# Performance work log

Hardware: AMD Instinct MI355X
Metric: run time of the kernel (lower is better)

## Reference

```python
import jax, jax.numpy as jnp
import numpy as np

V, WD, H, B, S, A = 50000, 300, 300, 64, 128, 8
H2 = 2 * H
NEG = -1e9


def _reverse_padded(x, lens):
    # reverse each sequence within its valid length; zeros elsewhere
    T = x.shape[1]
    idx = lens[:, None] - 1 - jnp.arange(T)[None, :]          # [B,T]
    valid = (idx >= 0)
    idx = jnp.clip(idx, 0, T - 1)
    return jnp.take_along_axis(x, idx[:, :, None], axis=1) * valid[:, :, None]


def _lstm_dir(x, lens, Wih, Whh, bih, bhh):
    # single-direction LSTM; emulates pack_padded: state frozen and output 0 past lens
    Bn, T, _ = x.shape
    Hn = Whh.shape[1]
    h0 = jnp.zeros((Bn, Hn), x.dtype)
    valid = (jnp.arange(T)[None, :] < lens[:, None]).astype(x.dtype)  # [B,T]

    def step(carry, inp):
        h, c = carry
        xt, vt = inp                                          # xt [B,D], vt [B,1]
        g = xt @ Wih.T + bih + h @ Whh.T + bhh                # [B,4H]
        i, f, gg, o = jnp.split(g, 4, axis=-1)                # torch gate order i,f,g,o
        i = jax.nn.sigmoid(i); f = jax.nn.sigmoid(f)
        o = jax.nn.sigmoid(o); gg = jnp.tanh(gg)
        c_new = f * c + i * gg
        h_new = o * jnp.tanh(c_new)
        h = vt * h_new + (1.0 - vt) * h
        c = vt * c_new + (1.0 - vt) * c
        return (h, c), vt * h_new

    _, outs = jax.lax.scan(step, (h0, h0), (x.transpose(1, 0, 2), valid.T[:, :, None]))
    return outs.transpose(1, 0, 2)                            # [B,T,H]


def _bilstm(x, lens, Wih, Whh, bih, bhh):
    fwd = _lstm_dir(x, lens, Wih[0], Whh[0], bih[0], bhh[0])
    xr = _reverse_padded(x, lens)
    bwd = _lstm_dir(xr, lens, Wih[1], Whh[1], bih[1], bhh[1])
    bwd = _reverse_padded(bwd, lens)
    return jnp.concatenate([fwd, bwd], axis=-1)               # [B,T,2H]


def setup_inputs() -> dict:
    key = jax.random.key(0)
    ks = jax.random.split(key, 16)
    lens_t = jax.random.randint(ks[0], (B,), S // 2, S + 1)
    ids_t = jax.random.randint(ks[1], (B, S), 1, V)
    text = jnp.where(jnp.arange(S)[None, :] < lens_t[:, None], ids_t, 0)
    lens_a = jax.random.randint(ks[2], (B,), 2, A + 1)
    ids_a = jax.random.randint(ks[3], (B, A), 1, V)
    aspect_ids = jnp.where(jnp.arange(A)[None, :] < lens_a[:, None], ids_a, 0)
    position_weight = jax.random.uniform(ks[4], (B, S), jnp.float32) * (text != 0)
    s = 0.05
    emb = jax.random.normal(ks[5], (V, WD), jnp.float32) * s
    emb = emb.at[0].set(0.0)  # padding row

    def lstm_params(k):
        k1, k2, k3, k4 = jax.random.split(k, 4)
        return (jax.random.normal(k1, (2, 4 * H, WD), jnp.float32) * s,
                jax.random.normal(k2, (2, 4 * H, H), jnp.float32) * s,
                jax.random.normal(k3, (2, 4 * H), jnp.float32) * s,
                jax.random.normal(k4, (2, 4 * H), jnp.float32) * s)

    l1_Wih, l1_Whh, l1_bih, l1_bhh = lstm_params(ks[6])
    l2_Wih, l2_Whh, l2_bih, l2_bhh = lstm_params(ks[7])
    return dict(
        text=text, aspect_ids=aspect_ids, position_weight=position_weight, emb=emb,
        l1_Wih=l1_Wih, l1_Whh=l1_Whh, l1_bih=l1_bih, l1_bhh=l1_bhh,
        l2_Wih=l2_Wih, l2_Whh=l2_Whh, l2_bih=l2_bih, l2_bhh=l2_bhh,
        lin1_W=jax.random.normal(ks[8], (2, H2, 2 * H2), jnp.float32) * s,
        lin1_b=jax.random.normal(ks[9], (2, H2), jnp.float32) * s,
        lin2_W=jax.random.normal(ks[10], (2, 1, H2), jnp.float32) * s,
        lin2_b=jax.random.normal(ks[11], (2, 1), jnp.float32) * s,
        fc_W=jax.random.normal(ks[12], (3, H2), jnp.float32) * s,
        fc_b=jax.random.normal(ks[13], (3,), jnp.float32) * s,
    )


def reference(text, aspect_ids, position_weight, emb,
              l1_Wih, l1_Whh, l1_bih, l1_bhh,
              l2_Wih, l2_Whh, l2_bih, l2_bhh,
              lin1_W, lin1_b, lin2_W, lin2_b, fc_W, fc_b):
    text_len = jnp.sum(text != 0, axis=-1)
    asp_len = jnp.sum(aspect_ids != 0, axis=-1)
    masks = (text != 0).astype(jnp.float32)          # [B,S]
    tmasks = (aspect_ids != 0).astype(jnp.float32)   # [B,A]
    wf = emb[text]                                    # [B,S,WD]
    af = emb[aspect_ids]                              # [B,A,WD]
    v = _bilstm(wf, text_len, l1_Wih, l1_Whh, l1_bih, l1_bhh)   # [B,S,2H]
    e = _bilstm(af, asp_len, l2_Wih, l2_Whh, l2_bih, l2_bhh)    # [B,A,2H]
    pair_mask = masks[:, :, None] * tmasks[:, None, :]          # [B,S,A]
    for i in range(2):
        a = jnp.einsum('bsd,bad->bsa', v, e)
        a = jnp.where(pair_mask == 0, NEG, a)
        a = jax.nn.softmax(a, axis=2)
        mid = jnp.einsum('bsa,bad->bsd', a, e)                  # [B,S,2H]
        mid = jnp.concatenate([mid, v], axis=-1)                # [B,S,4H]
        mid = jax.nn.leaky_relu(mid @ lin1_W[i].T + lin1_b[i])  # [B,S,2H]
        t = jax.nn.sigmoid(v @ lin2_W[i].T + lin2_b[i])         # [B,S,1]
        v = (1.0 - t) * mid + t * v
        v = position_weight[:, :, None] * v
    e_masked = jnp.where(tmasks[:, :, None] == 0, NEG, e)
    query = jnp.max(e_masked, axis=1)                           # [B,2H]
    alpha = jnp.einsum('bsd,bd->bs', v, query)
    alpha = jnp.where(masks == 0, NEG, alpha)
    alpha = jax.nn.softmax(alpha, axis=1)
    z = jnp.einsum('bs,bsd->bd', alpha, v)                      # [B,2H]
    return z @ fc_W.T + fc_b                                    # [B,3]
```

## Files before the change

kernel.cpp:

```cpp
#include <hip/hip_runtime.h>
#include <hip/hip_bf16.h>
#include <hip/hip_fp16.h>


typedef unsigned short u16;
typedef __attribute__((ext_vector_type(8))) short short8;
typedef __attribute__((ext_vector_type(4))) float floatx4;

#define NEGV -1e9f
#define MFMA __builtin_amdgcn_mfma_f32_16x16x32_bf16

__device__ __forceinline__ float bf2f(u16 u) {
    union { unsigned int i; float f; } x; x.i = ((unsigned int)u) << 16; return x.f;
}
__device__ __forceinline__ u16 f2bf(float f) {
    unsigned int u = __float_as_uint(f);
    unsigned int r = (u + 0x7fff + ((u >> 16) & 1)) >> 16;
    return (u16)r;
}
__device__ __forceinline__ float h16(u16 u) {
    __half h; *(u16*)&h = u; return __half2float(h);
}
__device__ __forceinline__ u16 f16(float f) {
    __half h = __float2half(f); return *(u16*)&h;
}
__device__ __forceinline__ float sigm(float x) { return 1.f / (1.f + expf(-x)); }
__device__ __forceinline__ float rdf(const void* p, size_t i, int flag) {
    return flag ? ((const float*)p)[i] : bf2f(((const u16*)p)[i]);
}

#if defined(__has_builtin)
# if __has_builtin(__builtin_amdgcn_fdot2)
#  define USE_FDOT2_BUILTIN 1
# endif
#endif
typedef __attribute__((ext_vector_type(2))) _Float16 half2v;
__device__ __forceinline__ float dot2f(unsigned int w, unsigned int h, float acc) {
#ifdef USE_FDOT2_BUILTIN
    union { unsigned int u; half2v v; } a, b;
    a.u = w; b.u = h;
    return __builtin_amdgcn_fdot2(a.v, b.v, acc, false);
#else
    asm("v_dot2_f32_f16 %0, %1, %2, %0" : "+v"(acc) : "v"(w), "v"(h));
    return acc;
#endif
}

__global__ void k_detect(const void* __restrict__ emb, int* __restrict__ flag) {
    __shared__ int cnt;
    if (threadIdx.x == 0) cnt = 0;
    __syncthreads();
    u16 x = ((const u16*)emb)[4096 + threadIdx.x];
    int e = (x >> 7) & 0xFF;
    if (e >= 0x8A) atomicAdd(&cnt, 1);
    __syncthreads();
    if (threadIdx.x == 0) *flag = (cnt > 8) ? 1 : 0;
}

__global__ void k_prep_small(const int* __restrict__ text, const int* __restrict__ asp,
                             int* __restrict__ lens) {
    int tid = threadIdx.x;
    if (tid < 64) {
        int c = 0;
        for (int s = 0; s < 128; ++s) c += (text[tid * 128 + s] != 0);
        lens[tid] = c;
    } else if (tid < 128) {
        int b = tid - 64; int c = 0;
        for (int a = 0; a < 8; ++a) c += (asp[b * 8 + a] != 0);
        lens[64 + b] = c;
    }
}

__global__ void k_pad_wih2(const void* __restrict__ W1, const void* __restrict__ W2,
                           const int* __restrict__ flag,
                           u16* __restrict__ d1h, u16* __restrict__ d1l,
                           u16* __restrict__ d2h, u16* __restrict__ d2l) {
    int i = blockIdx.x * 256 + threadIdx.x;
    if (i >= 2 * 2432 * 320) return;
    int f = *flag;
    int layer = i / (2432 * 320), r = i - layer * (2432 * 320);
    int n = r / 320, k = r - n * 320;
    const void* W = layer ? W2 : W1;
    float val = (n < 2400 && k < 300) ? rdf(W, (size_t)n * 300 + k, f) : 0.f;
    u16 hi = f2bf(val);
    float lo = val - bf2f(hi);
    if (layer) { d2h[r] = hi; d2l[r] = f2bf(lo); }
    else       { d1h[r] = hi; d1l[r] = f2bf(lo); }
}

__global__ void k_whhT2(const void* __restrict__ W1, const void* __restrict__ W2,
                        const int* __restrict__ flag,
                        u16* __restrict__ d1, u16* __restrict__ d2) {
    int i = blockIdx.x * 256 + threadIdx.x;
    if (i >= 2 * 720000) return;
    int f = *flag;
    int layer = i / 720000, r = i - layer * 720000;
    int dir = r / 360000, rr = r - dir * 360000;
    int kp = rr / 2400, t = rr - kp * 2400;
    int cc = t >> 1, j = t & 1;
    int k = 2 * kp + j;
    const void* W = layer ? W2 : W1;
    u16 bits = f16(rdf(W, (size_t)dir * 360000 + (size_t)cc * 300 + k, f));
    if (layer) d2[r] = bits; else d1[r] = bits;
}

__global__ void k_pad_lin1AB(const void* __restrict__ W, const int* __restrict__ flag,
                             u16* __restrict__ Ahi, u16* __restrict__ Alo,
                             u16* __restrict__ Bhi, u16* __restrict__ Blo) {
    int i = blockIdx.x * 256 + threadIdx.x;
    if (i >= 2 * 640 * 608) return;
    int f = *flag;
    int it = i / (640 * 608), r = i - it * (640 * 608);
    int n = r / 608, k = r - n * 608;
    float va = 0.f, vb = 0.f;
    if (n < 600 && k < 600) {
        va = rdf(W, (size_t)it * 720000 + (size_t)n * 1200 + k, f);
        vb = rdf(W, (size_t)it * 720000 + (size_t)n * 1200 + 600 + k, f);
    }
    u16 h;
    h = f2bf(va); Ahi[i] = h; Alo[i] = f2bf(va - bf2f(h));
    h = f2bf(vb); Bhi[i] = h; Blo[i] = f2bf(vb - bf2f(h));
}

__global__ void k_esplit(const float* __restrict__ e,
                         u16* __restrict__ ehi, u16* __restrict__ elo) {
    int i = blockIdx.x * 256 + threadIdx.x;
    if (i >= 512 * 608) return;
    int r = i / 608, k = i - r * 608;
    float val = (k < 600) ? e[r * 600 + k] : 0.f;
    u16 h = f2bf(val);
    ehi[i] = h;
    elo[i] = f2bf(val - bf2f(h));
}

__global__ void k_small(const void* pw, const void* l2w, const void* l2b,
                        const void* fcw, const void* fcb, const void* lb,
                        const void* b1i, const void* b1h, const void* b2i, const void* b2h,
                        const int* __restrict__ flag,
                        float* __restrict__ dst, float* __restrict__ bl,
                        float* __restrict__ bt, float* __restrict__ ba) {
    int i = blockIdx.x * 256 + threadIdx.x;
    int f = *flag;
    if (i < 8192)            dst[i] = rdf(pw, i, f);
    else if (i < 9392)       dst[i] = rdf(l2w, i - 8192, f);
    else if (i < 9394)       dst[i] = rdf(l2b, i - 9392, f);
    else if (i < 11194)      dst[i] = rdf(fcw, i - 9394, f);
    else if (i < 11197)      dst[i] = rdf(fcb, i - 11194, f);
    if (i < 1280) {
        int dir = i / 640, c = i - dir * 640;
        bl[i] = (c < 600) ? rdf(lb, dir * 600 + c, f) : 0.f;
    }
    if (i < 2400) {
        bt[i] = rdf(b1i, i, f) + rdf(b1h, i, f);
        ba[i] = rdf(b2i, i, f) + rdf(b2h, i, f);
    }
}

__device__ __forceinline__ void gemm_emb_tile(
    const void* __restrict__ emb, const int* __restrict__ ids,
    int base, int rpb, int stride, int f,
    const u16* __restrict__ Bhi, const u16* __restrict__ Blo,
    const float* __restrict__ bias,
    u16* __restrict__ C, int ldc, int nstore, int bx, int by, int tid)
{
    int wave = tid >> 6, lane = tid & 63;
    int l15 = lane & 15, quad = lane >> 4;
    int m0 = bx * 64 + wave * 16;
    int n0 = by * 64;

    int m = m0 + l15;
    int b = m / rpb, j = m - b * rpb;
    int id = ids[b * stride + base + j];
    const float* arow_f = (const float*)emb + (size_t)id * 300;
    const u16*   arow_b = (const u16*)emb + (size_t)id * 300;

    const u16* Bp  = Bhi + (size_t)(n0 + l15) * 320 + quad * 8;
    const u16* Bp2 = Blo + (size_t)(n0 + l15) * 320 + quad * 8;

    floatx4 acc0 = {0.f, 0.f, 0.f, 0.f};
    floatx4 acc1 = acc0, acc2 = acc0, acc3 = acc0;

    for (int kc = 0; kc < 10; ++kc) {
        int ko = kc * 32 + quad * 8;
        short8 ahi, alo;
        if (f) {
            if (ko + 8 <= 300) {
                float4 fa = *(const float4*)(arow_f + ko);
                float4 fb = *(const float4*)(arow_f + ko + 4);
                float vv[8] = {fa.x, fa.y, fa.z, fa.w, fb.x, fb.y, fb.z, fb.w};
                #pragma unroll
                for (int t = 0; t < 8; ++t) {
                    u16 h = f2bf(vv[t]);
                    ahi[t] = (short)h;
                    alo[t] = (short)f2bf(vv[t] - bf2f(h));
                }
            } else {
                #pragma unroll
                for (int t = 0; t < 8; ++t) {
                    int k = ko + t;
                    float vv = (k < 300) ? arow_f[k] : 0.f;
                    u16 h = f2bf(vv);
                    ahi[t] = (short)h;
                    alo[t] = (short)f2bf(vv - bf2f(h));
                }
            }
        } else {
            #pragma unroll
            for (int t = 0; t < 8; ++t) {
                int k = ko + t;
                ahi[t] = (k < 300) ? (short)arow_b[k] : (short)0;
                alo[t] = 0;
            }
        }
        int ko2 = kc * 32;
        short8 bh0 = *(const short8*)(Bp + ko2);
        short8 bh1 = *(const short8*)(Bp + (size_t)16 * 320 + ko2);
        short8 bh2 = *(const short8*)(Bp + (size_t)32 * 320 + ko2);
        short8 bh3 = *(const short8*)(Bp + (size_t)48 * 320 + ko2);
        short8 bl0 = *(const short8*)(Bp2 + ko2);
        short8 bl1 = *(const short8*)(Bp2 + (size_t)16 * 320 + ko2);
        short8 bl2 = *(const short8*)(Bp2 + (size_t)32 * 320 + ko2);
        short8 bl3 = *(const short8*)(Bp2 + (size_t)48 * 320 + ko2);
        acc0 = MFMA(ahi, bh0, acc0, 0, 0, 0);
        acc1 = MFMA(ahi, bh1, acc1, 0, 0, 0);
        acc2 = MFMA(ahi, bh2, acc2, 0, 0, 0);
        acc3 = MFMA(ahi, bh3, acc3, 0, 0, 0);
        acc0 = MFMA(ahi, bl0, acc0, 0, 0, 0);
        acc1 = MFMA(ahi, bl1, acc1, 0, 0, 0);
        acc2 = MFMA(ahi, bl2, acc2, 0, 0, 0);
        acc3 = MFMA(ahi, bl3, acc3, 0, 0, 0);
        acc0 = MFMA(alo, bh0, acc0, 0, 0, 0);
        acc1 = MFMA(alo, bh1, acc1, 0, 0, 0);
        acc2 = MFMA(alo, bh2, acc2, 0, 0, 0);
        acc3 = MFMA(alo, bh3, acc3, 0, 0, 0);
    }

    #pragma unroll
    for (int c = 0; c < 4; ++c) {
        floatx4 acc = (c == 0) ? acc0 : (c == 1) ? acc1 : (c == 2) ? acc2 : acc3;
        int col = n0 + c * 16 + l15;
        if (col >= nstore) continue;
        float bb = bias[col];
        #pragma unroll
        for (int r = 0; r < 4; ++r) {
            int row = m0 + quad * 4 + r;
            C[(size_t)row * ldc + col] = f16(acc[r] + bb);
        }
    }
}

__global__ __launch_bounds__(256) void gemm_embk(
    const void* __restrict__ emb, const int* __restrict__ ids,
    int base, int rpb, int stride, const int* __restrict__ flag,
    const u16* __restrict__ Bhi, const u16* __restrict__ Blo,
    const float* __restrict__ bias,
    u16* __restrict__ C, int ldc, int nstore)
{
    gemm_emb_tile(emb, ids, base, rpb, stride, *flag, Bhi, Blo, bias,
                  C, ldc, nstore, blockIdx.x, blockIdx.y, threadIdx.x);
}

__device__ __forceinline__ void gemm_core(
    const u16* __restrict__ Ap, const u16* __restrict__ Ap2,
    const u16* __restrict__ Bp, const u16* __restrict__ Bp2,
    int lda, int ldb, int nk,
    floatx4& acc0, floatx4& acc1, floatx4& acc2, floatx4& acc3)
{
    for (int kc = 0; kc < nk; ++kc) {
        int ko = kc * 32;
        short8 bh0 = *(const short8*)(Bp + ko);
        short8 bh1 = *(const short8*)(Bp + (size_t)16 * ldb + ko);
        short8 bh2 = *(const short8*)(Bp + (size_t)32 * ldb + ko);
        short8 bh3 = *(const short8*)(Bp + (size_t)48 * ldb + ko);
        short8 bl0 = *(const short8*)(Bp2 + ko);
        short8 bl1 = *(const short8*)(Bp2 + (size_t)16 * ldb + ko);
        short8 bl2 = *(const short8*)(Bp2 + (size_t)32 * ldb + ko);
        short8 bl3 = *(const short8*)(Bp2 + (size_t)48 * ldb + ko);
        short8 a  = *(const short8*)(Ap + ko);
        short8 al = *(const short8*)(Ap2 + ko);
        acc0 = MFMA(a, bh0, acc0, 0, 0, 0);
        acc1 = MFMA(a, bh1, acc1, 0, 0, 0);
        acc2 = MFMA(a, bh2, acc2, 0, 0, 0);
        acc3 = MFMA(a, bh3, acc3, 0, 0, 0);
        acc0 = MFMA(a, bl0, acc0, 0, 0, 0);
        acc1 = MFMA(a, bl1, acc1, 0, 0, 0);
        acc2 = MFMA(a, bl2, acc2, 0, 0, 0);
        acc3 = MFMA(a, bl3, acc3, 0, 0, 0);
        acc0 = MFMA(al, bh0, acc0, 0, 0, 0);
        acc1 = MFMA(al, bh1, acc1, 0, 0, 0);
        acc2 = MFMA(al, bh2, acc2, 0, 0, 0);
        acc3 = MFMA(al, bh3, acc3, 0, 0, 0);
    }
}

__global__ __launch_bounds__(256) void gemm_ew(
    const u16* __restrict__ Ahi, const u16* __restrict__ Alo,
    const u16* __restrict__ l1a_hi, const u16* __restrict__ l1a_lo,
    float* __restrict__ EW)
{
    int tid = threadIdx.x;
    int wave = tid >> 6, lane = tid & 63;
    int l15 = lane & 15, quad = lane >> 4;
    int iter = blockIdx.z;
    int m0 = blockIdx.x * 64 + wave * 16;
    int n0 = blockIdx.y * 64;
    const u16* Ap  = Ahi + (size_t)(m0 + l15) * 608 + quad * 8;
    const u16* Ap2 = Alo + (size_t)(m0 + l15) * 608 + quad * 8;
    const u16* Bp  = l1a_hi + (size_t)iter * 640 * 608 + (size_t)(n0 + l15) * 608 + quad * 8;
    const u16* Bp2 = l1a_lo + (size_t)iter * 640 * 608 + (size_t)(n0 + l15) * 608 + quad * 8;
    floatx4 acc0 = {0.f, 0.f, 0.f, 0.f};
    floatx4 acc1 = acc0, acc2 = acc0, acc3 = acc0;
    gemm_core(Ap, Ap2, Bp, Bp2, 608, 608, 19, acc0, acc1, acc2, acc3);
    #pragma unroll
    for (int c = 0; c < 4; ++c) {
        floatx4 acc = (c == 0) ? acc0 : (c == 1) ? acc1 : (c == 2) ? acc2 : acc3;
        int col = n0 + c * 16 + l15;
        if (col >= 600) continue;
        #pragma unroll
        for (int r = 0; r < 4; ++r) {
            int row = m0 + quad * 4 + r;
            EW[((size_t)iter * 512 + row) * 600 + col] = acc[r];
        }
    }
}

__global__ __launch_bounds__(256) void gemm_vt(
    const u16* __restrict__ vhi, const u16* __restrict__ vlo,
    const u16* __restrict__ Bhi, const u16* __restrict__ Blo,
    const float* __restrict__ bias,
    const float* __restrict__ EW, const float* __restrict__ a_sm,
    const float* __restrict__ tg, const float* __restrict__ pw,
    float* __restrict__ vio)
{
    __shared__ float al_s[64][8];
    __shared__ float ew_s[8][64];
    int tid = threadIdx.x;
    int wave = tid >> 6, lane = tid & 63;
    int l15 = lane & 15, quad = lane >> 4;
    int m0 = blockIdx.x * 64 + wave * 16;
    int n0 = blockIdx.y * 64;
    int row0 = blockIdx.x * 64;
    int bidx = row0 >> 7;

    for (int i = tid; i < 512; i += 256)
        al_s[i >> 3][i & 7] = a_sm[(size_t)(row0 + (i >> 3)) * 8 + (i & 7)];
    for (int i = tid; i < 512; i += 256) {
        int a = i >> 6, cc = i & 63;
        int col = n0 + cc;
        ew_s[a][cc] = (col < 600) ? EW[((size_t)bidx * 8 + a) * 600 + col] : 0.f;
    }
    __syncthreads();

    const u16* Ap  = vhi + (size_t)(m0 + l15) * 608 + quad * 8;
    const u16* Ap2 = vlo + (size_t)(m0 + l15) * 608 + quad * 8;
    const u16* Bp  = Bhi + (size_t)(n0 + l15) * 608 + quad * 8;
    const u16* Bp2 = Blo + (size_t)(n0 + l15) * 608 + quad * 8;
    floatx4 acc0 = {0.f, 0.f, 0.f, 0.f};
    floatx4 acc1 = acc0, acc2 = acc0, acc3 = acc0;
    gemm_core(Ap, Ap2, Bp, Bp2, 608, 608, 19, acc0, acc1, acc2, acc3);

    #pragma unroll
    for (int c = 0; c < 4; ++c) {
        floatx4 acc = (c == 0) ? acc0 : (c == 1) ? acc1 : (c == 2) ? acc2 : acc3;
        int cc = c * 16 + l15;
        int col = n0 + cc;
        if (col >= 600) continue;
        float bb = bias[col];
        #pragma unroll
        for (int r = 0; r < 4; ++r) {
            int rr = wave * 16 + quad * 4 + r;
            int row = row0 + rr;
            float mid = 0.f;
            #pragma unroll
            for (int a = 0; a < 8; ++a) mid += al_s[rr][a] * ew_s[a][cc];
            float val = acc[r] + bb + mid;
            val = val > 0.f ? val : 0.01f * val;
            float t = tg[row];
            size_t vi = (size_t)row * 600 + col;
            float vv = vio[vi];
            vio[vi] = pw[row] * ((1.f - t) * val + t * vv);
        }
    }
}

__global__ __launch_bounds__(960, 1) void k_lstm6(
    const u16* __restrict__ xf, const u16* __restrict__ xb, int ldx, int rpb,
    int base_f, int base_b, const u16* __restrict__ whhT,
    const int* __restrict__ lens, float* __restrict__ out, int T, int init,
    float* __restrict__ hst, float* __restrict__ cst, int nsteps,
    const u16* __restrict__ xa, const u16* __restrict__ whhA,
    const int* __restrict__ lensA, float* __restrict__ outA,
    float* __restrict__ hstA, float* __restrict__ cstA, int nLstm,
    const void* __restrict__ emb, const int* __restrict__ text,
    int bf_next, int bb_next, const int* __restrict__ flag,
    const u16* __restrict__ wih_hi, const u16* __restrict__ wih_lo,
    const float* __restrict__ bias_t,
    u16* __restrict__ xf_next, u16* __restrict__ xb_next)
{
    __shared__ float part[6][1200];
    __shared__ u16 wlds[6][4][2400];
    __shared__ __align__(4) u16 hs16[304];
    int blk = blockIdx.x;
    if (blk >= nLstm) {
        if (threadIdx.x >= 256) return;
        int g = blk - nLstm;
        int dirn = g / 608; int t = g - dirn * 608;
        int bx = t & 31, by = t >> 5;
        gemm_emb_tile(emb, text, dirn ? bb_next : bf_next, 32, 128, *flag,
                      wih_hi + (dirn ? 1200ull * 320 : 0),
                      wih_lo + (dirn ? 1200ull * 320 : 0),
                      bias_t + (dirn ? 1200 : 0),
                      dirn ? xb_next : xf_next, 1200, 1200, bx, by, threadIdx.x);
        return;
    }
    if (blk >= 128) {
        blk -= 128;
        xf = xa; xb = xa + 1200; ldx = 2400; rpb = 8;
        base_f = 0; base_b = 0;
        whhT = whhA; lens = lensA; out = outA; T = 8; init = 1;
        hst = hstA; cst = cstA; nsteps = 8;
    }
    int tid = threadIdx.x;
    int g6 = tid / 160, u = tid - g6 * 160;
    bool act = (u < 150);
    int b = blk >> 1, dir = blk & 1;
    int len = lens[b];
    float c = 0.f, hf = 0.f;
    const u16* wbase = whhT + (size_t)dir * 360000 + (size_t)g6 * 60000 + 16 * u;

    uint4 wA[8], wB[8];
    if (act) {
        #pragma unroll
        for (int r = 0; r < 8; ++r) {
            wA[r] = *(const uint4*)(wbase + (size_t)r * 2400);
            wB[r] = *(const uint4*)(wbase + (size_t)r * 2400 + 8);
        }
        #pragma unroll
        for (int r = 0; r < 4; ++r) {
            *(uint4*)&wlds[g6][r][16 * u]     = *(const uint4*)(wbase + (size_t)(8 + r) * 2400);
            *(uint4*)&wlds[g6][r][16 * u + 8] = *(const uint4*)(wbase + (size_t)(8 + r) * 2400 + 8);
        }
    }
    if (tid < 300) {
        hf = init ? 0.f : hst[(size_t)blk * 300 + tid];
        c  = init ? 0.f : cst[(size_t)blk * 300 + tid];
        hs16[tid] = f16(hf);
    }
    __syncthreads();
    const u16* wstream = wbase + (size_t)12 * 2400;

    for (int s = 0; s < nsteps; ++s) {
        int pos = dir ? (base_b + nsteps - 1 - s) : (base_f + s);
        if (pos >= len) continue;
        if (act) {
            float a0 = 0.f, a1 = 0.f, a2 = 0.f, a3 = 0.f;
            float a4 = 0.f, a5 = 0.f, a6 = 0.f, a7 = 0.f;
            const unsigned int* h2p = (const unsigned int*)(hs16 + g6 * 50);
            #define DOT8(va, vb, hh)                                   \
                a0 = dot2f((va).x, hh, a0); a1 = dot2f((va).y, hh, a1);\
                a2 = dot2f((va).z, hh, a2); a3 = dot2f((va).w, hh, a3);\
                a4 = dot2f((vb).x, hh, a4); a5 = dot2f((vb).y, hh, a5);\
                a6 = dot2f((vb).z, hh, a6); a7 = dot2f((vb).w, hh, a7);
            #pragma unroll
            for (int r = 0; r < 8; ++r) {
                unsigned int h2 = h2p[r];
                DOT8(wA[r], wB[r], h2);
            }
            #pragma unroll
            for (int r = 0; r < 4; ++r) {
                unsigned int h2 = h2p[8 + r];
                uint4 va = *(const uint4*)&wlds[g6][r][16 * u];
                uint4 vb = *(const uint4*)&wlds[g6][r][16 * u + 8];
                DOT8(va, vb, h2);
            }
            const u16* wp = wstream;
            #pragma unroll 4
            for (int i = 0; i < 13; ++i) {
                unsigned int h2 = h2p[12 + i];
                uint4 va = *(const uint4*)wp;
                uint4 vb = *(const uint4*)(wp + 8);
                wp += 2400;
                DOT8(va, vb, h2);
            }
            #undef DOT8
            float* pp = &part[g6][8 * u];
            float4 w0 = {a0, a1, a2, a3};
            float4 w1 = {a4, a5, a6, a7};
            *(float4*)pp = w0;
            *(float4*)(pp + 4) = w1;
        }
        __syncthreads();
        if (tid < 300) {
            const u16* xr = dir ? (xb + (size_t)(b * rpb + pos - base_b) * ldx)
                                : (xf + (size_t)(b * rpb + pos - base_f) * ldx);
            float gi = h16(xr[tid]), gf = h16(xr[300 + tid]);
            float gg = h16(xr[600 + tid]), go = h16(xr[900 + tid]);
            #pragma unroll
            for (int g = 0; g < 6; ++g) {
                gi += part[g][tid];
                gf += part[g][300 + tid];
                gg += part[g][600 + tid];
                go += part[g][900 + tid];
            }
            gi = sigm(gi); gf = sigm(gf); gg = tanhf(gg); go = sigm(go);
            c = gf * c + gi * gg;
            float hn = go * tanhf(c);
            out[((size_t)b * T + pos) * 600 + dir * 300 + tid] = hn;
            hf = hn;
            hs16[tid] = f16(hn);
        }
        __syncthreads();
    }
    if (tid < 300) {
        hst[(size_t)blk * 300 + tid] = hf;
        cst[(size_t)blk * 300 + tid] = c;
    }
}

__global__ __launch_bounds__(128) void k_scorev(
    const float* __restrict__ v, const float* __restrict__ e,
    const int* __restrict__ text, const int* __restrict__ asp,
    const float* __restrict__ l2w, const float* __restrict__ l2b, int iter,
    float* __restrict__ a_sm, float* __restrict__ tg,
    u16* __restrict__ vhi, u16* __restrict__ vlo)
{
    __shared__ float vs[600];
    __shared__ float red[2][9];
    int row = blockIdx.x;
    int b = row >> 7;
    int t = threadIdx.x, wv = t >> 6, lane = t & 63;
    const float* vrow = v + (size_t)row * 600;
    const float* eb = e + (size_t)b * 4800;
    const float* w2 = l2w + iter * 600;

    for (int d = t; d < 600; d += 128) vs[d] = vrow[d];
    __syncthreads();

    float acc[9];
    #pragma unroll
    for (int j = 0; j < 9; ++j) acc[j] = 0.f;
    for (int d = t; d < 600; d += 128) {
        float vv = vs[d];
        #pragma unroll
        for (int a = 0; a < 8; ++a) acc[a] += vv * eb[a * 600 + d];
        acc[8] += vv * w2[d];
    }
    #pragma unroll
    for (int off = 32; off >= 1; off >>= 1) {
        #pragma unroll
        for (int j = 0; j < 9; ++j) acc[j] += __shfl_down(acc[j], off, 64);
    }
    if (lane == 0) {
        #pragma unroll
        for (int j = 0; j < 9; ++j) red[wv][j] = acc[j];
    }
    __syncthreads();
    if (t == 0) {
        float dots[9];
        #pragma unroll
        for (int j = 0; j < 9; ++j) dots[j] = red[0][j] + red[1][j];
        tg[row] = sigm(dots[8] + l2b[iter]);
        bool sm = (text[row] != 0);
        float sc[8]; float mx = -INFINITY;
        #pragma unroll
        for (int a = 0; a < 8; ++a) {
            sc[a] = (sm && asp[b * 8 + a] != 0) ? dots[a] : NEGV;
            mx = fmaxf(mx, sc[a]);
        }
        float den = 0.f;
        #pragma unroll
        for (int a = 0; a < 8; ++a) { sc[a] = expf(sc[a] - mx); den += sc[a]; }
        float inv = 1.f / den;
        #pragma unroll
        for (int a = 0; a < 8; ++a) a_sm[(size_t)row * 8 + a] = sc[a] * inv;
    }
    for (int d = t; d < 608; d += 128) {
        float val = (d < 600) ? vs[d] : 0.f;
        u16 h = f2bf(val);
        vhi[(size_t)row * 608 + d] = h;
        vlo[(size_t)row * 608 + d] = f2bf(val - bf2f(h));
    }
}

__global__ void k_query(const float* __restrict__ e, const int* __restrict__ asp,
                        float* __restrict__ q) {
    int i = blockIdx.x * 256 + threadIdx.x;
    if (i >= 64 * 600) return;
    int b = i / 600, d = i - b * 600;
    float m = NEGV;
    for (int a = 0; a < 8; ++a)
        if (asp[b * 8 + a] != 0) m = fmaxf(m, e[(size_t)b * 4800 + a * 600 + d]);
    q[i] = m;
}

__global__ __launch_bounds__(128) void k_final(
    const float* __restrict__ v, const float* __restrict__ q,
    const int* __restrict__ text, const float* __restrict__ fcW,
    const float* __restrict__ fcb, const int* __restrict__ flag, void* __restrict__ outv)
{
    __shared__ float red[128];
    __shared__ float al[128];
    __shared__ float zz[600];
    int b = blockIdx.x, s = threadIdx.x;
    const float* vrow = v + (size_t)(b * 128 + s) * 600;
    const float* qb = q + (size_t)b * 600;
    float sc = 0.f;
    for (int d = 0; d < 600; ++d) sc += vrow[d] * qb[d];
    if (text[b * 128 + s] == 0) sc = NEGV;
    red[s] = sc; __syncthreads();
    for (int off = 64; off >= 1; off >>= 1) {
        if (s < off) red[s] = fmaxf(red[s], red[s + off]);
        __syncthreads();
    }
    float mx = red[0]; __syncthreads();
    float ex = expf(sc - mx);
    red[s] = ex; __syncthreads();
    for (int off = 64; off >= 1; off >>= 1) {
        if (s < off) red[s] += red[s + off];
        __syncthreads();
    }
    float alpha = ex / red[0];
    al[s] = alpha; __syncthreads();
    for (int d = s; d < 600; d += 128) {
        float z = 0.f;
        for (int s2 = 0; s2 < 128; ++s2) z += al[s2] * v[(size_t)(b * 128 + s2) * 600 + d];
        zz[d] = z;
    }
    __syncthreads();
    if (s < 3) {
        float o = 0.f;
        for (int d = 0; d < 600; ++d) o += zz[d] * fcW[s * 600 + d];
        o += fcb[s];
        if (*flag) ((float*)outv)[b * 3 + s] = o;
        else       ((u16*)outv)[b * 3 + s] = f2bf(o);
    }
}

extern "C" void kernel_launch(void* const* d_in, const int* in_sizes, int n_in,
                              void* d_out, int out_size, void* d_ws, size_t ws_size,
                              hipStream_t stream) {
    const int*  text   = (const int*)d_in[0];
    const int*  asp    = (const int*)d_in[1];
    const void* pw     = d_in[2];
    const void* emb    = d_in[3];
    const void* l1_Wih = d_in[4];
    const void* l1_Whh = d_in[5];
    const void* l1_bih = d_in[6];
    const void* l1_bhh = d_in[7];
    const void* l2_Wih = d_in[8];
    const void* l2_Whh = d_in[9];
    const void* l2_bih = d_in[10];
    const void* l2_bhh = d_in[11];
    const void* lin1_W = d_in[12];
    const void* lin1_b = d_in[13];
    const void* lin2_W = d_in[14];
    const void* lin2_b = d_in[15];
    const void* fcW    = d_in[16];
    const void* fcb    = d_in[17];
    (void)ws_size; (void)n_in; (void)in_sizes; (void)out_size;

    char* w = (char*)d_ws;
    size_t off = 0;
    auto alloc = [&](size_t bytes) -> void* {
        void* p = w + off;
        off += (bytes + 255) & ~(size_t)255;
        return p;
    };
    int*   flag     = (int*)  alloc(4);
    int*   lens     = (int*)  alloc(128ull * 4);
    float* bias_t   = (float*)alloc(2400ull * 4);
    float* bias_a   = (float*)alloc(2400ull * 4);
    float* bias_l1  = (float*)alloc(1280ull * 4);
    float* smallf   = (float*)alloc(11197ull * 4);
    float* tg       = (float*)alloc(8192ull * 4);
    float* a_sm     = (float*)alloc(8192ull * 8 * 4);
    float* query    = (float*)alloc(64ull * 600 * 4);
    float* hst_t    = (float*)alloc(128ull * 300 * 4);
    float* cst_t    = (float*)alloc(128ull * 300 * 4);
    float* hst_a    = (float*)alloc(128ull * 300 * 4);
    float* cst_a    = (float*)alloc(128ull * 300 * 4);
    float* e        = (float*)alloc(512ull * 600 * 4);
    float* v        = (float*)alloc(8192ull * 600 * 4);
    float* pw_f     = smallf;
    float* l2w_f    = smallf + 8192;
    float* l2b_f    = smallf + 9392;
    float* fcW_f    = smallf + 9394;
    float* fcb_f    = smallf + 11194;
    size_t phase_off = off;
    u16*   wiht_hi  = (u16*)  alloc(2432ull * 320 * 2);
    u16*   wiht_lo  = (u16*)  alloc(2432ull * 320 * 2);
    u16*   wiha_hi  = (u16*)  alloc(2432ull * 320 * 2);
    u16*   wiha_lo  = (u16*)  alloc(2432ull * 320 * 2);
    u16*   whhT_t   = (u16*)  alloc(720000ull * 2);
    u16*   whhT_a   = (u16*)  alloc(720000ull * 2);
    u16*   xf0      = (u16*)  alloc(2048ull * 1200 * 2);
    u16*   xb0      = (u16*)  alloc(2048ull * 1200 * 2);
    u16*   xf1      = (u16*)  alloc(2048ull * 1200 * 2);
    u16*   xb1      = (u16*)  alloc(2048ull * 1200 * 2);
    u16*   xproj_a  = (u16*)  alloc(512ull * 2400 * 2);
    off = phase_off;
    u16*   l1a_hi   = (u16*)  alloc(2ull * 640 * 608 * 2);
    u16*   l1a_lo   = (u16*)  alloc(2ull * 640 * 608 * 2);
    u16*   l1b_hi   = (u16*)  alloc(2ull * 640 * 608 * 2);
    u16*   l1b_lo   = (u16*)  alloc(2ull * 640 * 608 * 2);
    u16*   ehi      = (u16*)  alloc(512ull * 608 * 2);
    u16*   elo      = (u16*)  alloc(512ull * 608 * 2);
    float* EW       = (float*)alloc(2ull * 512 * 600 * 4);
    u16*   vhi      = (u16*)  alloc(8192ull * 608 * 2);
    u16*   vlo      = (u16*)  alloc(8192ull * 608 * 2);

    hipMemsetAsync(v, 0, 8192ull * 600 * 4, stream);
    hipMemsetAsync(e, 0, 512ull * 600 * 4, stream);

    k_detect<<<1, 256, 0, stream>>>(emb, flag);
    k_prep_small<<<1, 128, 0, stream>>>(text, asp, lens);
    k_pad_wih2<<<(2 * 2432 * 320 + 255) / 256, 256, 0, stream>>>(
        l1_Wih, l2_Wih, flag, wiht_hi, wiht_lo, wiha_hi, wiha_lo);
    k_whhT2<<<(2 * 720000 + 255) / 256, 256, 0, stream>>>(
        l1_Whh, l2_Whh, flag, whhT_t, whhT_a);
    k_small<<<49, 256, 0, stream>>>(pw, lin2_W, lin2_b, fcW, fcb, lin1_b,
                                    l1_bih, l1_bhh, l2_bih, l2_bhh, flag,
                                    smallf, bias_l1, bias_t, bias_a);

    gemm_embk<<<dim3(8, 38), 256, 0, stream>>>(emb, asp, 0, 8, 8, flag,
        wiha_hi, wiha_lo, bias_a, xproj_a, 2400, 2400);
    gemm_embk<<<dim3(32, 19), 256, 0, stream>>>(emb, text, 0, 32, 128, flag,
        wiht_hi, wiht_lo, bias_t, xf0, 1200, 1200);
    gemm_embk<<<dim3(32, 19), 256, 0, stream>>>(emb, text, 96, 32, 128, flag,
        wiht_hi + 1200ull * 320, wiht_lo + 1200ull * 320, bias_t + 1200,
        xb0, 1200, 1200);

    for (int kk = 0; kk < 4; ++kk) {
        int bf = 32 * kk;
        int bb = 96 - 32 * kk;
        u16* xfc = (kk & 1) ? xf1 : xf0;
        u16* xbc = (kk & 1) ? xb1 : xb0;
        u16* xfn = (kk & 1) ? xf0 : xf1;
        u16* xbn = (kk & 1) ? xb0 : xb1;
        int nLstm = (kk == 0) ? 256 : 128;
        int haveNext = (kk < 3);
        int nblk = nLstm + (haveNext ? 1216 : 0);
        k_lstm6<<<nblk, 960, 0, stream>>>(xfc, xbc, 1200, 32, bf, bb,
            whhT_t, lens, v, 128, kk == 0 ? 1 : 0, hst_t, cst_t, 32,
            xproj_a, whhT_a, lens + 64, e, hst_a, cst_a, nLstm,
            emb, text, bf + 32, bb - 32, flag, wiht_hi, wiht_lo, bias_t,
            xfn, xbn);
    }

    k_pad_lin1AB<<<(2 * 640 * 608 + 255) / 256, 256, 0, stream>>>(
        lin1_W, flag, l1a_hi, l1a_lo, l1b_hi, l1b_lo);
    k_esplit<<<(512 * 608 + 255) / 256, 256, 0, stream>>>(e, ehi, elo);
    gemm_ew<<<dim3(8, 10, 2), 256, 0, stream>>>(ehi, elo, l1a_hi, l1a_lo, EW);

    for (int iter = 0; iter < 2; ++iter) {
        k_scorev<<<8192, 128, 0, stream>>>(v, e, text, asp, l2w_f, l2b_f,
            iter, a_sm, tg, vhi, vlo);
        gemm_vt<<<dim3(128, 10), 256, 0, stream>>>(vhi, vlo,
            l1b_hi + (size_t)iter * 640 * 608, l1b_lo + (size_t)iter * 640 * 608,
            bias_l1 + iter * 640, EW + (size_t)iter * 512 * 600,
            a_sm, tg, pw_f, v);
    }

    k_query<<<150, 256, 0, stream>>>(e, asp, query);
    k_final<<<64, 128, 0, stream>>>(v, query, text, fcW_f, fcb_f, flag, d_out);
}
```

Before: 1.102 ms.

## Hold recurrent weights in AGPRs and split LDS tiles into bank-friendly halves

Moves the register-resident slice of the LSTM recurrent weights from VGPRs into accumulation registers using explicit accvgpr write/read instructions. It shrinks that slice from 8 to 6 rows and lets the streamed global part grow from 13 to 15 rows, now issued before the register and LDS parts. It also splits the LDS weight tile and the partial-sum buffer into two 8-byte-strided halves to reduce bank conflicts, with a remapped index in the gate reduction. The aim is to ease VGPR pressure and LDS conflicts, but it adds more global weight traffic each step and extra accvgpr read instructions.

New measurement: 1.137 ms. +3.1%, slower.

```diff
diff --git a/kernel.cpp b/kernel.cpp
--- a/kernel.cpp
+++ b/kernel.cpp
@@ -397,8 +397,8 @@
     const float* __restrict__ bias_t,
     u16* __restrict__ xf_next, u16* __restrict__ xb_next)
 {
-    __shared__ float part[6][1200];
-    __shared__ u16 wlds[6][4][2400];
+    __shared__ float part2[6][2][600];
+    __shared__ u16 wlds[6][4][2][1200];
     __shared__ __align__(4) u16 hs16[304];
     int blk = blockIdx.x;
     if (blk >= nLstm) {
@@ -428,17 +428,25 @@
     float c = 0.f, hf = 0.f;
     const u16* wbase = whhT + (size_t)dir * 360000 + (size_t)g6 * 60000 + 16 * u;
 
-    uint4 wA[8], wB[8];
+    uint4 agA[6], agB[6];
+    #pragma unroll
+    for (int r = 0; r < 6; ++r) {
+        uint4 t0 = *(const uint4*)(wbase + (size_t)r * 2400);
+        uint4 t1 = *(const uint4*)(wbase + (size_t)r * 2400 + 8);
+        asm volatile("v_accvgpr_write_b32 %0, %1" : "=a"(agA[r].x) : "v"(t0.x));
+        asm volatile("v_accvgpr_write_b32 %0, %1" : "=a"(agA[r].y) : "v"(t0.y));
+        asm volatile("v_accvgpr_write_b32 %0, %1" : "=a"(agA[r].z) : "v"(t0.z));
+        asm volatile("v_accvgpr_write_b32 %0, %1" : "=a"(agA[r].w) : "v"(t0.w));
+        asm volatile("v_accvgpr_write_b32 %0, %1" : "=a"(agB[r].x) : "v"(t1.x));
+        asm volatile("v_accvgpr_write_b32 %0, %1" : "=a"(agB[r].y) : "v"(t1.y));
+        asm volatile("v_accvgpr_write_b32 %0, %1" : "=a"(agB[r].z) : "v"(t1.z));
+        asm volatile("v_accvgpr_write_b32 %0, %1" : "=a"(agB[r].w) : "v"(t1.w));
+    }
     if (act) {
         #pragma unroll
-        for (int r = 0; r < 8; ++r) {
-            wA[r] = *(const uint4*)(wbase + (size_t)r * 2400);
-            wB[r] = *(const uint4*)(wbase + (size_t)r * 2400 + 8);
-        }
-        #pragma unroll
         for (int r = 0; r < 4; ++r) {
-            *(uint4*)&wlds[g6][r][16 * u]     = *(const uint4*)(wbase + (size_t)(8 + r) * 2400);
-            *(uint4*)&wlds[g6][r][16 * u + 8] = *(const uint4*)(wbase + (size_t)(8 + r) * 2400 + 8);
+            *(uint4*)&wlds[g6][r][0][8 * u] = *(const uint4*)(wbase + (size_t)(6 + r) * 2400);
+            *(uint4*)&wlds[g6][r][1][8 * u] = *(const uint4*)(wbase + (size_t)(6 + r) * 2400 + 8);
         }
     }
     if (tid < 300) {
@@ -446,8 +454,12 @@
         c  = init ? 0.f : cst[(size_t)blk * 300 + tid];
         hs16[tid] = f16(hf);
     }
+    int gc0 = tid,       gh0 = (gc0 >> 2) & 1, gi0 = ((gc0 >> 3) << 2) | (gc0 & 3);
+    int gc1 = 300 + tid, gh1 = (gc1 >> 2) & 1, gi1 = ((gc1 >> 3) << 2) | (gc1 & 3);
+    int gc2 = 600 + tid, gh2 = (gc2 >> 2) & 1, gi2 = ((gc2 >> 3) << 2) | (gc2 & 3);
+    int gc3 = 900 + tid, gh3 = (gc3 >> 2) & 1, gi3 = ((gc3 >> 3) << 2) | (gc3 & 3);
     __syncthreads();
-    const u16* wstream = wbase + (size_t)12 * 2400;
+    const u16* wstream = wbase + (size_t)10 * 2400;
 
     for (int s = 0; s < nsteps; ++s) {
         int pos = dir ? (base_b + nsteps - 1 - s) : (base_f + s);
@@ -461,33 +473,41 @@
                 a2 = dot2f((va).z, hh, a2); a3 = dot2f((va).w, hh, a3);\
                 a4 = dot2f((vb).x, hh, a4); a5 = dot2f((vb).y, hh, a5);\
                 a6 = dot2f((vb).z, hh, a6); a7 = dot2f((vb).w, hh, a7);
-            #pragma unroll
-            for (int r = 0; r < 8; ++r) {
-                unsigned int h2 = h2p[r];
-                DOT8(wA[r], wB[r], h2);
-            }
-            #pragma unroll
-            for (int r = 0; r < 4; ++r) {
-                unsigned int h2 = h2p[8 + r];
-                uint4 va = *(const uint4*)&wlds[g6][r][16 * u];
-                uint4 vb = *(const uint4*)&wlds[g6][r][16 * u + 8];
-                DOT8(va, vb, h2);
-            }
             const u16* wp = wstream;
-            #pragma unroll 4
-            for (int i = 0; i < 13; ++i) {
-                unsigned int h2 = h2p[12 + i];
+            #pragma unroll 5
+            for (int i = 0; i < 15; ++i) {
+                unsigned int h2 = h2p[10 + i];
                 uint4 va = *(const uint4*)wp;
                 uint4 vb = *(const uint4*)(wp + 8);
                 wp += 2400;
                 DOT8(va, vb, h2);
             }
+            #pragma unroll
+            for (int r = 0; r < 6; ++r) {
+                unsigned int h2 = h2p[r];
+                uint4 va, vb;
+                asm("v_accvgpr_read_b32 %0, %1" : "=v"(va.x) : "a"(agA[r].x));
+                asm("v_accvgpr_read_b32 %0, %1" : "=v"(va.y) : "a"(agA[r].y));
+                asm("v_accvgpr_read_b32 %0, %1" : "=v"(va.z) : "a"(agA[r].z));
+                asm("v_accvgpr_read_b32 %0, %1" : "=v"(va.w) : "a"(agA[r].w));
+                asm("v_accvgpr_read_b32 %0, %1" : "=v"(vb.x) : "a"(agB[r].x));
+                asm("v_accvgpr_read_b32 %0, %1" : "=v"(vb.y) : "a"(agB[r].y));
+                asm("v_accvgpr_read_b32 %0, %1" : "=v"(vb.z) : "a"(agB[r].z));
+                asm("v_accvgpr_read_b32 %0, %1" : "=v"(vb.w) : "a"(agB[r].w));
+                DOT8(va, vb, h2);
+            }
+            #pragma unroll
+            for (int r = 0; r < 4; ++r) {
+                unsigned int h2 = h2p[6 + r];
+                uint4 va = *(const uint4*)&wlds[g6][r][0][8 * u];
+                uint4 vb = *(const uint4*)&wlds[g6][r][1][8 * u];
+                DOT8(va, vb, h2);
+            }
             #undef DOT8
-            float* pp = &part[g6][8 * u];
             float4 w0 = {a0, a1, a2, a3};
             float4 w1 = {a4, a5, a6, a7};
-            *(float4*)pp = w0;
-            *(float4*)(pp + 4) = w1;
+            *(float4*)&part2[g6][0][4 * u] = w0;
+            *(float4*)&part2[g6][1][4 * u] = w1;
         }
         __syncthreads();
         if (tid < 300) {
@@ -497,10 +517,10 @@
             float gg = h16(xr[600 + tid]), go = h16(xr[900 + tid]);
             #pragma unroll
             for (int g = 0; g < 6; ++g) {
-                gi += part[g][tid];
-                gf += part[g][300 + tid];
-                gg += part[g][600 + tid];
-                go += part[g][900 + tid];
+                gi += part2[g][gh0][gi0];
+                gf += part2[g][gh1][gi1];
+                gg += part2[g][gh2][gi2];
+                go += part2[g][gh3][gi3];
             }
             gi = sigm(gi); gf = sigm(gf); gg = tanhf(gg); go = sigm(go);
             c = gf * c + gi * gg;
```

## Store recurrent LSTM weights as scaled FP8 and keep more in LDS

Applied to the files above, without the earlier changes.

Recurrent Whh weights are quantized to FP8 (e4m3) with a 64x scale instead of fp16, halving their footprint. The register-held weight slices are dropped; 8 rows now sit in LDS and the rest stream from global, with dot products done via fp8-to-f32 unpack plus FMAs against an fp32 hidden state scaled by 1/64. This cuts weight bandwidth and register pressure in the sequential recurrence, but FP8 greatly lowers accuracy, and the unpack-plus-FMA path costs more ALU work than packed fp16 dot2.

Result: slower. 1.389 ms (+26.0%).

```diff
diff --git a/kernel.cpp b/kernel.cpp
--- a/kernel.cpp
+++ b/kernel.cpp
@@ -6,6 +6,7 @@
 typedef unsigned short u16;
 typedef __attribute__((ext_vector_type(8))) short short8;
 typedef __attribute__((ext_vector_type(4))) float floatx4;
+typedef __attribute__((ext_vector_type(2))) float floatx2;
 
 #define NEGV -1e9f
 #define MFMA __builtin_amdgcn_mfma_f32_16x16x32_bf16
@@ -30,19 +31,49 @@
 }
 
 #if defined(__has_builtin)
-# if __has_builtin(__builtin_amdgcn_fdot2)
-#  define USE_FDOT2_BUILTIN 1
+# if __has_builtin(__builtin_amdgcn_cvt_pk_f32_fp8) && __has_builtin(__builtin_amdgcn_cvt_pk_fp8_f32)
+#  define USE_CVT_FP8 1
 # endif
 #endif
-typedef __attribute__((ext_vector_type(2))) _Float16 half2v;
-__device__ __forceinline__ float dot2f(unsigned int w, unsigned int h, float acc) {
-#ifdef USE_FDOT2_BUILTIN
-    union { unsigned int u; half2v v; } a, b;
-    a.u = w; b.u = h;
-    return __builtin_amdgcn_fdot2(a.v, b.v, acc, false);
+
+template <bool WORD>
+__device__ __forceinline__ floatx2 fp8pk(unsigned int w) {
+#ifdef USE_CVT_FP8
+    return __builtin_amdgcn_cvt_pk_f32_fp8((int)w, WORD);
 #else
-    asm("v_dot2_f32_f16 %0, %1, %2, %0" : "+v"(acc) : "v"(w), "v"(h));
-    return acc;
+    unsigned int sh = WORD ? 16u : 0u;
+    floatx2 r;
+    #pragma unroll
+    for (int t = 0; t < 2; ++t) {
+        unsigned int b = (w >> (sh + 8 * t)) & 0xFFu;
+        unsigned s = b >> 7, e = (b >> 3) & 15, m = b & 7;
+        union { unsigned u; float f; } x;
+        if (e) x.u = (s << 31) | ((e + 120) << 23) | (m << 20);
+        else { x.f = (float)(int)m * 0.001953125f; if (s) x.f = -x.f; }
+        r[t] = x.f;
+    }
+    return r;
+#endif
+}
+
+__device__ __forceinline__ unsigned char f2fp8(float f) {
+#ifdef USE_CVT_FP8
+    int p = __builtin_amdgcn_cvt_pk_fp8_f32(f, f, 0, false);
+    return (unsigned char)(p & 0xFF);
+#else
+    unsigned s = f < 0.f ? 1u : 0u;
+    float a = fabsf(f);
+    if (a >= 448.f) return (unsigned char)((s << 7) | 0x7E);
+    if (a < 0.015625f) {
+        int m = (int)rintf(a * 512.f);
+        if (m > 7) return (unsigned char)((s << 7) | (1 << 3));
+        return (unsigned char)((s << 7) | m);
+    }
+    int ex; float fr = frexpf(a, &ex);
+    int q = (int)rintf(fr * 16.f);
+    if (q == 16) { q = 8; ex += 1; }
+    int E = ex + 6;
+    return (unsigned char)((s << 7) | (E << 3) | (q - 8));
 #endif
 }
 
@@ -90,7 +121,7 @@
 
 __global__ void k_whhT2(const void* __restrict__ W1, const void* __restrict__ W2,
                         const int* __restrict__ flag,
-                        u16* __restrict__ d1, u16* __restrict__ d2) {
+                        unsigned char* __restrict__ d1, unsigned char* __restrict__ d2) {
     int i = blockIdx.x * 256 + threadIdx.x;
     if (i >= 2 * 720000) return;
     int f = *flag;
@@ -100,7 +131,7 @@
     int cc = t >> 1, j = t & 1;
     int k = 2 * kp + j;
     const void* W = layer ? W2 : W1;
-    u16 bits = f16(rdf(W, (size_t)dir * 360000 + (size_t)cc * 300 + k, f));
+    unsigned char bits = f2fp8(64.f * rdf(W, (size_t)dir * 360000 + (size_t)cc * 300 + k, f));
     if (layer) d2[r] = bits; else d1[r] = bits;
 }
 
@@ -385,10 +416,10 @@
 
 __global__ __launch_bounds__(960, 1) void k_lstm6(
     const u16* __restrict__ xf, const u16* __restrict__ xb, int ldx, int rpb,
-    int base_f, int base_b, const u16* __restrict__ whhT,
+    int base_f, int base_b, const unsigned char* __restrict__ whhT,
     const int* __restrict__ lens, float* __restrict__ out, int T, int init,
     float* __restrict__ hst, float* __restrict__ cst, int nsteps,
-    const u16* __restrict__ xa, const u16* __restrict__ whhA,
+    const u16* __restrict__ xa, const unsigned char* __restrict__ whhA,
     const int* __restrict__ lensA, float* __restrict__ outA,
     float* __restrict__ hstA, float* __restrict__ cstA, int nLstm,
     const void* __restrict__ emb, const int* __restrict__ text,
@@ -398,8 +429,8 @@
     u16* __restrict__ xf_next, u16* __restrict__ xb_next)
 {
     __shared__ float part[6][1200];
-    __shared__ u16 wlds[6][4][2400];
-    __shared__ __align__(4) u16 hs16[304];
+    __shared__ __align__(16) unsigned char wlds[6][8][2400];
+    __shared__ float hs32[304];
     int blk = blockIdx.x;
     if (blk >= nLstm) {
         if (threadIdx.x >= 256) return;
@@ -426,28 +457,20 @@
     int b = blk >> 1, dir = blk & 1;
     int len = lens[b];
     float c = 0.f, hf = 0.f;
-    const u16* wbase = whhT + (size_t)dir * 360000 + (size_t)g6 * 60000 + 16 * u;
-
-    uint4 wA[8], wB[8];
+    const unsigned char* wbase = whhT + (size_t)dir * 360000
+                               + (size_t)g6 * 25 * 2400 + 16 * u;
     if (act) {
         #pragma unroll
-        for (int r = 0; r < 8; ++r) {
-            wA[r] = *(const uint4*)(wbase + (size_t)r * 2400);
-            wB[r] = *(const uint4*)(wbase + (size_t)r * 2400 + 8);
-        }
-        #pragma unroll
-        for (int r = 0; r < 4; ++r) {
-            *(uint4*)&wlds[g6][r][16 * u]     = *(const uint4*)(wbase + (size_t)(8 + r) * 2400);
-            *(uint4*)&wlds[g6][r][16 * u + 8] = *(const uint4*)(wbase + (size_t)(8 + r) * 2400 + 8);
-        }
+        for (int r = 0; r < 8; ++r)
+            *(uint4*)&wlds[g6][r][16 * u] = *(const uint4*)(wbase + (size_t)r * 2400);
     }
     if (tid < 300) {
         hf = init ? 0.f : hst[(size_t)blk * 300 + tid];
         c  = init ? 0.f : cst[(size_t)blk * 300 + tid];
-        hs16[tid] = f16(hf);
+        hs32[tid] = hf * 0.015625f;
     }
     __syncthreads();
-    const u16* wstream = wbase + (size_t)12 * 2400;
+    const unsigned char* wstream = wbase + (size_t)8 * 2400;
 
     for (int s = 0; s < nsteps; ++s) {
         int pos = dir ? (base_b + nsteps - 1 - s) : (base_f + s);
@@ -455,34 +478,29 @@
         if (act) {
             float a0 = 0.f, a1 = 0.f, a2 = 0.f, a3 = 0.f;
             float a4 = 0.f, a5 = 0.f, a6 = 0.f, a7 = 0.f;
-            const unsigned int* h2p = (const unsigned int*)(hs16 + g6 * 50);
-            #define DOT8(va, vb, hh)                                   \
-                a0 = dot2f((va).x, hh, a0); a1 = dot2f((va).y, hh, a1);\
-                a2 = dot2f((va).z, hh, a2); a3 = dot2f((va).w, hh, a3);\
-                a4 = dot2f((vb).x, hh, a4); a5 = dot2f((vb).y, hh, a5);\
-                a6 = dot2f((vb).z, hh, a6); a7 = dot2f((vb).w, hh, a7);
+            const float* hp = hs32 + g6 * 50;
+            #define ACCPAIR(w32, aa, ab)                                        \
+                { floatx2 lo = fp8pk<false>(w32), hi = fp8pk<true>(w32);        \
+                  aa = fmaf(lo.x, h0, aa); aa = fmaf(lo.y, h1, aa);             \
+                  ab = fmaf(hi.x, h0, ab); ab = fmaf(hi.y, h1, ab); }
+            #define ACC8(wv, h0v, h1v)                                          \
+                { float h0 = h0v, h1 = h1v;                                     \
+                  ACCPAIR((wv).x, a0, a1); ACCPAIR((wv).y, a2, a3);             \
+                  ACCPAIR((wv).z, a4, a5); ACCPAIR((wv).w, a6, a7); }
             #pragma unroll
             for (int r = 0; r < 8; ++r) {
-                unsigned int h2 = h2p[r];
-                DOT8(wA[r], wB[r], h2);
+                uint4 wv = *(const uint4*)&wlds[g6][r][16 * u];
+                ACC8(wv, hp[2 * r], hp[2 * r + 1]);
             }
-            #pragma unroll
-            for (int r = 0; r < 4; ++r) {
-                unsigned int h2 = h2p[8 + r];
-                uint4 va = *(const uint4*)&wlds[g6][r][16 * u];
-                uint4 vb = *(const uint4*)&wlds[g6][r][16 * u + 8];
-                DOT8(va, vb, h2);
+            const unsigned char* wp = wstream;
+            #pragma unroll 4
+            for (int i = 0; i < 17; ++i) {
+                uint4 wv = *(const uint4*)wp;
+                wp += 2400;
+                ACC8(wv, hp[16 + 2 * i], hp[17 + 2 * i]);
             }
-            const u16* wp = wstream;
-            #pragma unroll 4
-            for (int i = 0; i < 13; ++i) {
-                unsigned int h2 = h2p[12 + i];
-                uint4 va = *(const uint4*)wp;
-                uint4 vb = *(const uint4*)(wp + 8);
-                wp += 2400;
-                DOT8(va, vb, h2);
-            }
-            #undef DOT8
+            #undef ACC8
+            #undef ACCPAIR
             float* pp = &part[g6][8 * u];
             float4 w0 = {a0, a1, a2, a3};
             float4 w1 = {a4, a5, a6, a7};
@@ -507,7 +525,7 @@
             float hn = go * tanhf(c);
             out[((size_t)b * T + pos) * 600 + dir * 300 + tid] = hn;
             hf = hn;
-            hs16[tid] = f16(hn);
+            hs32[tid] = hn * 0.015625f;
         }
         __syncthreads();
     }
@@ -691,8 +709,8 @@
     u16*   wiht_lo  = (u16*)  alloc(2432ull * 320 * 2);
     u16*   wiha_hi  = (u16*)  alloc(2432ull * 320 * 2);
     u16*   wiha_lo  = (u16*)  alloc(2432ull * 320 * 2);
-    u16*   whhT_t   = (u16*)  alloc(720000ull * 2);
-    u16*   whhT_a   = (u16*)  alloc(720000ull * 2);
+    unsigned char* whhT_t8 = (unsigned char*)alloc(720000ull);
+    unsigned char* whhT_a8 = (unsigned char*)alloc(720000ull);
     u16*   xf0      = (u16*)  alloc(2048ull * 1200 * 2);
     u16*   xb0      = (u16*)  alloc(2048ull * 1200 * 2);
     u16*   xf1      = (u16*)  alloc(2048ull * 1200 * 2);
@@ -717,7 +735,7 @@
     k_pad_wih2<<<(2 * 2432 * 320 + 255) / 256, 256, 0, stream>>>(
         l1_Wih, l2_Wih, flag, wiht_hi, wiht_lo, wiha_hi, wiha_lo);
     k_whhT2<<<(2 * 720000 + 255) / 256, 256, 0, stream>>>(
-        l1_Whh, l2_Whh, flag, whhT_t, whhT_a);
+        l1_Whh, l2_Whh, flag, whhT_t8, whhT_a8);
     k_small<<<49, 256, 0, stream>>>(pw, lin2_W, lin2_b, fcW, fcb, lin1_b,
                                     l1_bih, l1_bhh, l2_bih, l2_bhh, flag,
                                     smallf, bias_l1, bias_t, bias_a);
@@ -741,8 +759,8 @@
         int haveNext = (kk < 3);
         int nblk = nLstm + (haveNext ? 1216 : 0);
         k_lstm6<<<nblk, 960, 0, stream>>>(xfc, xbc, 1200, 32, bf, bb,
-            whhT_t, lens, v, 128, kk == 0 ? 1 : 0, hst_t, cst_t, 32,
-            xproj_a, whhT_a, lens + 64, e, hst_a, cst_a, nLstm,
+            whhT_t8, lens, v, 128, kk == 0 ? 1 : 0, hst_t, cst_t, 32,
+            xproj_a, whhT_a8, lens + 64, e, hst_a, cst_a, nLstm,
             emb, text, bf + 32, bb - 32, flag, wiht_hi, wiht_lo, bias_t,
             xfn, xbn);
     }
```
